# Kernel optimization log

Measured on AMD Instinct MI355X. Metric: run time of the kernel, lower is better.

Reference implementation:

```python
import jax, jax.numpy as jnp
import numpy as np

B, LV, D = 8, 4096, 256   # batch, temporal length, channels
N = 2048                   # total ROIs across the batch
P = 32                     # output_size (number of output bins)
G = int(np.ceil(LV / P))   # static max adaptive sampling grid (sampling_ratio=-1)


def setup_inputs() -> dict:
    key = jax.random.key(0)
    k1, k2, k3 = jax.random.split(key, 3)
    feat = jax.random.normal(k1, (B, LV, D), dtype=jnp.float32)
    # boxes: (start, end) along the lv axis, sorted so start <= end, in [0, LV)
    boxes = jnp.sort(
        jax.random.uniform(k2, (N, 2), dtype=jnp.float32, minval=0.0, maxval=float(LV)),
        axis=1,
    )
    batch_idx = jax.random.randint(k3, (N,), 0, B, dtype=jnp.int32)
    return {"feat": feat, "boxes": boxes, "batch_idx": batch_idx}


def _roi_align_1d(feat, boxes, batch_idx):
    # Faithful 1D specialization of torchvision roi_align with boxes
    # (0, y1, 1, y2), output_size=(P, 1), aligned=True, spatial_scale=1,
    # sampling_ratio=-1. The width axis contributes a single sample at x=0
    # with weight 1, so only the y (lv) axis math remains.
    feat_flat = feat.reshape(B * LV, D)
    y1, y2 = boxes[:, 0], boxes[:, 1]
    roi_h = y2 - y1                       # aligned=True: no max(., 1) clamp
    start = y1 - 0.5                      # aligned offset
    bin_h = roi_h / P                     # [N]
    grid_h = jnp.ceil(bin_h).astype(jnp.int32)          # adaptive samples per bin
    count = jnp.maximum(grid_h, 1).astype(feat.dtype)   # avg denominator
    sub = bin_h / jnp.maximum(grid_h, 1)                # spacing inside a bin [N]
    # bin start positions: [N, P]
    bin_off = start[:, None] + jnp.arange(P, dtype=feat.dtype)[None, :] * bin_h[:, None]
    base = batch_idx.astype(jnp.int32) * LV             # [N] row offset into feat_flat

    def bilinear(y):  # y: [N, P] -> [N, P, D]
        valid = (y >= -1.0) & (y <= float(LV))
        yc = jnp.maximum(y, 0.0)
        y_lo = jnp.floor(yc).astype(jnp.int32)
        hi_case = y_lo >= LV - 1
        y_lo = jnp.where(hi_case, LV - 1, y_lo)
        y_hi = jnp.where(hi_case, LV - 1, y_lo + 1)
        yc = jnp.where(hi_case, y_lo.astype(y.dtype), yc)
        ly = yc - y_lo.astype(y.dtype)
        v = (1.0 - ly)[..., None] * feat_flat[base[:, None] + y_lo] \
            + ly[..., None] * feat_flat[base[:, None] + y_hi]
        return jnp.where(valid[..., None], v, 0.0)

    def step(acc, g):
        y = bin_off + (g.astype(feat.dtype) + 0.5) * sub[:, None]   # [N, P]
        m = (g < grid_h)[:, None, None]                              # sample active?
        return acc + jnp.where(m, bilinear(y), 0.0), None

    acc0 = jnp.zeros((N, P, D), dtype=feat.dtype)
    acc, _ = jax.lax.scan(step, acc0, jnp.arange(G, dtype=jnp.int32))
    return acc / count[:, None, None]   # [N, P, D] (torch output after transpose(1,2))


def reference(feat, boxes, batch_idx):
    return _roi_align_1d(feat, boxes, batch_idx)
```

## Files before the change

### kernel.cpp

```cpp
#include <hip/hip_runtime.h>

#define B_     8
#define LV_    4096
#define D_     256
#define N_     2048
#define P_     32
#define WROWS_ 64
#define SEGS_  4
#define NWIN_  (B_ * (LV_ / WROWS_))
#define NBLK_  (NWIN_ * SEGS_)

typedef float v4f __attribute__((ext_vector_type(4)));

__device__ __forceinline__ float lane_bcast_f(float v, int l) {
    return __int_as_float(__builtin_amdgcn_readlane(__float_as_int(v), l));
}

__device__ __forceinline__ int bin_r_first(const float* __restrict__ boxes, int n, int p) {
    const float y1 = boxes[2 * n], y2 = boxes[2 * n + 1];
    const float bin_h = (y2 - y1) * (1.0f / (float)P_);
    const int gh = (int)ceilf(bin_h);
    if (gh < 1) return 0;
    const float sub  = bin_h / (float)gh;
    const float boff = (y1 - 0.5f) + (float)p * bin_h;
    const float a    = fmaf(0.5f, sub, boff);
    int r = (int)floorf(a);
    if (r < 0) r = 0;
    if (r > LV_ - 1) r = LV_ - 1;
    return r;
}

__global__ __launch_bounds__(256) void build_order_kernel(
    const int* __restrict__ batch_idx, int* __restrict__ order, int* __restrict__ offs)
{
    __shared__ int cnt[B_], cur[B_];
    const int tid = threadIdx.x;
    if (tid < B_) cnt[tid] = 0;
    __syncthreads();
    for (int n = tid; n < N_; n += 256) atomicAdd(&cnt[batch_idx[n]], 1);
    __syncthreads();
    if (tid == 0) {
        int s = 0;
        for (int b = 0; b < B_; ++b) { cur[b] = s; offs[b] = s; s += cnt[b]; }
        offs[B_] = s;
    }
    __syncthreads();
    for (int n = tid; n < N_; n += 256)
        order[atomicAdd(&cur[batch_idx[n]], 1)] = n;
}

__device__ __forceinline__ void process_bin(
    const float* __restrict__ feat, const float* __restrict__ boxes,
    const int* __restrict__ batch_idx, float* __restrict__ out,
    const v4f* tile, int wb, int wlo, int idx, int lane)
{
    const int n = idx >> 5, p = idx & 31;
    const int bi = __builtin_amdgcn_readfirstlane(batch_idx[n]);

    const float y1 = boxes[2 * n], y2 = boxes[2 * n + 1];
    const float bin_h = (y2 - y1) * (1.0f / (float)P_);
    const int gh = (int)ceilf(bin_h);

    const v4f* prow = (const v4f*)feat + (long)bi * (LV_ * (D_ / 4));
    v4f acc0 = {0.f,0.f,0.f,0.f}, acc1 = {0.f,0.f,0.f,0.f};

    if (gh >= 1) {
        const float cntf = (float)gh, sub = bin_h / cntf, inv_sub = 1.0f / sub;
        const float halfsub = 0.5f * sub;
        const float boff = (y1 - 0.5f) + (float)p * bin_h;
        const float a = fmaf(0.5f, sub, boff), ylast = fmaf(cntf - 0.5f, sub, boff);

        int r_first = (int)floorf(a);
        if (r_first < 0) r_first = 0; if (r_first > LV_-1) r_first = LV_-1;
        int r_last = (int)floorf(ylast) + 1;
        if (r_last > LV_-1) r_last = LV_-1; if (r_last < r_first) r_last = r_first;
        const int r0 = __builtin_amdgcn_readfirstlane(r_first);
        const int rl = __builtin_amdgcn_readfirstlane(r_last);
        const float lanef = (float)lane;

        for (int gbase = r0; gbase <= rl; gbase += 64) {
            int kmax = rl - gbase; if (kmax > 63) kmax = 63;

            const int   r  = gbase + lane;
            const float d0 = ((float)gbase + lanef) - a;
            const float dm = d0 - 1.0f, dp = d0 + 1.0f;
            const float nm = fminf(fmaxf(ceilf(dm * inv_sub), 0.0f), cntf);
            const float n0 = fminf(fmaxf(ceilf(d0 * inv_sub), 0.0f), cntf);
            const float np = fminf(fmaxf(ceilf(dp * inv_sub), 0.0f), cntf);
            float Pm = fmaf(nm, dm, -halfsub * fmaf(nm, nm, -nm));
            float P0 = fmaf(n0, d0, -halfsub * fmaf(n0, n0, -n0));
            float Pp = fmaf(np, dp, -halfsub * fmaf(np, np, -np));
            if (r == 0)       Pm = P0;
            if (r == LV_ - 1) Pp = P0 + cntf;
            const float Wl = (Pm + Pp) - 2.0f * P0;

            const int t = kmax + 1;
            int lo, hi;
            if (tile && bi == wb) {
                lo = wlo - gbase;          lo = lo < 0 ? 0 : (lo > t ? t : lo);
                hi = wlo + WROWS_ - gbase; hi = hi < lo ? lo : (hi > t ? t : hi);
            } else { lo = t; hi = t; }

#define GSEG(KS, KE) do {                                                        \
    int k = (KS);                                                                \
    const v4f* pS = prow + (long)(gbase + k) * (D_ / 4);                         \
    for (; k + 4 <= (KE); k += 4) {                                              \
        v4f v0 = pS[lane], v1 = pS[lane+64], v2 = pS[lane+128], v3 = pS[lane+192];\
        acc0 += v0 * lane_bcast_f(Wl, k);   acc1 += v1 * lane_bcast_f(Wl, k+1);  \
        acc0 += v2 * lane_bcast_f(Wl, k+2); acc1 += v3 * lane_bcast_f(Wl, k+3);  \
        pS += 4 * (D_ / 4); }                                                    \
    for (; k < (KE); ++k) { v4f v = pS[lane]; acc0 += v * lane_bcast_f(Wl, k); pS += (D_ / 4); } \
} while (0)

            GSEG(0, lo);
            {
                int k = lo;
                const v4f* tp = tile + (gbase + lo - wlo) * 64 + lane;
                for (; k + 4 <= hi; k += 4) {
                    v4f t0 = tp[0], t1 = tp[64], t2 = tp[128], t3 = tp[192];
                    acc0 += t0 * lane_bcast_f(Wl, k);   acc1 += t1 * lane_bcast_f(Wl, k+1);
                    acc0 += t2 * lane_bcast_f(Wl, k+2); acc1 += t3 * lane_bcast_f(Wl, k+3);
                    tp += 256;
                }
                for (; k < hi; ++k) { acc0 += tp[0] * lane_bcast_f(Wl, k); tp += 64; }
            }
            GSEG(hi, t);
#undef GSEG
        }
    }

    const float inv_c = 1.0f / (float)(gh > 1 ? gh : 1);
    v4f res = (acc0 + acc1) * inv_c;
    v4f* op = (v4f*)out + ((long)n * P_ + p) * (D_ / 4) + lane;
    __builtin_nontemporal_store(res, op);
}

__global__ __launch_bounds__(512) void roi_win_kernel(
    const float* __restrict__ feat, const float* __restrict__ boxes,
    const int* __restrict__ batch_idx, const int* __restrict__ order,
    const int* __restrict__ offs, float* __restrict__ out)
{
    __shared__ v4f tile[WROWS_ * 64];
    __shared__ int flag;

    const int tid  = threadIdx.x;
    const int lane = tid & 63;
    const int wv   = tid >> 6;
    const int bid  = blockIdx.x;

    const int blk = (bid & 7) * (NBLK_ / 8) + (bid >> 3);
    const int w   = blk >> 2;
    const int seg = blk & (SEGS_ - 1);
    const int wb  = w >> 6;
    const int wt  = w & 63;
    const int wlo = wt << 6;

    const int off_b = offs[wb];
    const int cnt_b = offs[wb + 1] - off_b;

    if (tid == 0) flag = 0;
    __syncthreads();
    for (int jj = tid; jj < cnt_b; jj += 512) {
        const int n = order[off_b + jj];
        const int rlo = bin_r_first(boxes, n, 0);
        const int rhi = bin_r_first(boxes, n, P_ - 1);
        if (rlo < wlo + WROWS_ && rhi >= wlo) { flag = 1; break; }
    }
    __syncthreads();
    if (!flag) return;

    {
        const int r0 = wv * 8;
        const float* srow = feat + ((long)wb * LV_ + wlo + r0) * D_ + lane * 4;
        v4f* lrow = tile + r0 * 64;
#if __has_builtin(__builtin_amdgcn_global_load_lds)
        #pragma unroll
        for (int j = 0; j < 8; ++j) {
            __builtin_amdgcn_global_load_lds(
                (const __attribute__((address_space(1))) void*)(srow + j * D_),
                (__attribute__((address_space(3))) void*)(lrow + j * 64),
                16, 0, 0);
        }
#else
        const v4f* src = (const v4f*)feat + ((long)wb * LV_ + wlo + r0) * (D_ / 4) + lane;
        v4f t0 = src[0],   t1 = src[64],  t2 = src[128], t3 = src[192];
        v4f t4 = src[256], t5 = src[320], t6 = src[384], t7 = src[448];
        v4f* dst = lrow + lane;
        dst[0]   = t0; dst[64]  = t1; dst[128] = t2; dst[192] = t3;
        dst[256] = t4; dst[320] = t5; dst[384] = t6; dst[448] = t7;
#endif
    }
    __syncthreads();

    for (int j = seg + SEGS_ * wv; j < cnt_b; j += SEGS_ * 8) {
        const int n = __builtin_amdgcn_readfirstlane(order[off_b + j]);

        const float y1 = boxes[2 * n], y2 = boxes[2 * n + 1];
        const float bin_h = (y2 - y1) * (1.0f / (float)P_);
        const int gh = (int)ceilf(bin_h);

        int pl_c, width;
        if (bin_h > 1e-6f) {
            const float sub   = bin_h / (float)(gh < 1 ? 1 : gh);
            const float A0    = (y1 - 0.5f) + 0.5f * sub;
            const float invbh = 1.0f / bin_h;
            const float plf = (wt == 0)  ? 0.0f  : ((float)wlo - A0) * invbh - 1.0f;
            const float phf = (wt == 63) ? 32.0f : ((float)(wlo + WROWS_) - A0) * invbh + 1.0f;
            int pl = (int)floorf(fminf(fmaxf(plf, 0.0f), 32.0f));
            int ph = (int)ceilf(fminf(fmaxf(phf, 0.0f), 32.0f));
            if (ph < pl) ph = pl;
            pl_c = pl; width = ph - pl;
        } else {
            pl_c = 0; width = 32;
        }
        if (width == 0) continue;

        bool in = false;
        if (lane < width) {
            const int p = pl_c + lane;
            in = ((bin_r_first(boxes, n, p) >> 6) == wt);
        }
        const unsigned long long m = __ballot(in);
        if (!m) continue;
        const int pl   = pl_c + __builtin_ctzll(m);
        const int pcnt = __builtin_popcountll(m);

        for (int pp = pl; pp < pl + pcnt; ++pp)
            process_bin(feat, boxes, batch_idx, out, tile, wb, wlo, (n << 5) | pp, lane);
    }
}

__global__ __launch_bounds__(256) void roi_plain_kernel(
    const float* __restrict__ feat, const float* __restrict__ boxes,
    const int* __restrict__ batch_idx, float* __restrict__ out)
{
    const int slot = blockIdx.x * 4 + (threadIdx.x >> 6);
    const int lane = threadIdx.x & 63;
    process_bin(feat, boxes, batch_idx, out, nullptr, 0, 0, slot, lane);
}

extern "C" void kernel_launch(void* const* d_in, const int* in_sizes, int n_in,
                              void* d_out, int out_size, void* d_ws, size_t ws_size,
                              hipStream_t stream) {
    const float* feat      = (const float*)d_in[0];
    const float* boxes     = (const float*)d_in[1];
    const int*   batch_idx = (const int*)d_in[2];
    float*       out       = (float*)d_out;

    if (ws_size >= (size_t)(N_ + B_ + 1) * sizeof(int)) {
        int* order = (int*)d_ws;
        int* offs  = order + N_;
        build_order_kernel<<<1, 256, 0, stream>>>(batch_idx, order, offs);
        roi_win_kernel<<<NBLK_, 512, 0, stream>>>(feat, boxes, batch_idx, order, offs, out);
    } else {
        roi_plain_kernel<<<(N_ * P_) / 4, 256, 0, stream>>>(feat, boxes, batch_idx, out);
    }
}
```

Measured before the change: 203.6 us.

## Build compacted per-window bin list in LDS for balanced wave scheduling

Each window block now enumerates every (ROI, bin) pair of its batch and counts those whose first sample row lands in the window. It prefix-sums the counts across waves and writes a compact list of bin indices into LDS. Waves then take entries from that list in stride, so work is spread per bin instead of per ROI, replacing the earlier flag prefilter and per-ROI range ballot. The cost is a doubled full scan of 32 bins per ROI for every block, and a fallback global-memory path when the list would exceed its LDS capacity.

```diff
diff --git a/kernel.cpp b/kernel.cpp
--- a/kernel.cpp
+++ b/kernel.cpp
@@ -9,6 +9,7 @@
 #define SEGS_  4
 #define NWIN_  (B_ * (LV_ / WROWS_))
 #define NBLK_  (NWIN_ * SEGS_)
+#define LCAP_  4096
 
 typedef float v4f __attribute__((ext_vector_type(4)));
 
@@ -141,7 +142,8 @@
     const int* __restrict__ offs, float* __restrict__ out)
 {
     __shared__ v4f tile[WROWS_ * 64];
-    __shared__ int flag;
+    __shared__ unsigned short list[LCAP_];
+    __shared__ int wsum[9];
 
     const int tid  = threadIdx.x;
     const int lane = tid & 63;
@@ -155,19 +157,55 @@
     const int wt  = w & 63;
     const int wlo = wt << 6;
 
-    const int off_b = offs[wb];
-    const int cnt_b = offs[wb + 1] - off_b;
-
-    if (tid == 0) flag = 0;
-    __syncthreads();
-    for (int jj = tid; jj < cnt_b; jj += 512) {
-        const int n = order[off_b + jj];
-        const int rlo = bin_r_first(boxes, n, 0);
-        const int rhi = bin_r_first(boxes, n, P_ - 1);
-        if (rlo < wlo + WROWS_ && rhi >= wlo) { flag = 1; break; }
-    }
-    __syncthreads();
-    if (!flag) return;
+    const int off_b  = offs[wb];
+    const int cnt_b  = offs[wb + 1] - off_b;
+    const int npairs = cnt_b * 32;
+
+    int c = 0;
+    for (int q = tid; q < npairs; q += 512) {
+        const int n = order[off_b + (q >> 5)];
+        if ((bin_r_first(boxes, n, q & 31) >> 6) == wt) ++c;
+    }
+    int sc = c;
+    #pragma unroll
+    for (int d = 1; d < 64; d <<= 1) {
+        const int v = __shfl_up(sc, d);
+        if (lane >= d) sc += v;
+    }
+    if (lane == 63) wsum[wv] = sc;
+    __syncthreads();
+    if (tid == 0) {
+        int s = 0;
+        for (int i = 0; i < 8; ++i) { const int t = wsum[i]; wsum[i] = s; s += t; }
+        wsum[8] = s;
+    }
+    __syncthreads();
+    const int K = wsum[8];
+    if (K == 0) return;
+
+    if (K > LCAP_) {
+        const int slot = seg * 8 + wv;
+        for (int j = slot; j < cnt_b; j += 32) {
+            const int n = __builtin_amdgcn_readfirstlane(order[off_b + j]);
+            bool in = false;
+            if (lane < 32) in = ((bin_r_first(boxes, n, lane) >> 6) == wt);
+            unsigned long long m = __ballot(in);
+            while (m) {
+                const int p = __builtin_ctzll(m);
+                m &= m - 1;
+                process_bin(feat, boxes, batch_idx, out, nullptr, 0, 0, (n << 5) | p, lane);
+            }
+        }
+        return;
+    }
+
+    int o = wsum[wv] + (sc - c);
+    for (int q = tid; q < npairs; q += 512) {
+        const int n = order[off_b + (q >> 5)];
+        const int p = q & 31;
+        if ((bin_r_first(boxes, n, p) >> 6) == wt)
+            list[o++] = (unsigned short)((n << 5) | p);
+    }
 
     {
         const int r0 = wv * 8;
@@ -192,41 +230,9 @@
     }
     __syncthreads();
 
-    for (int j = seg + SEGS_ * wv; j < cnt_b; j += SEGS_ * 8) {
-        const int n = __builtin_amdgcn_readfirstlane(order[off_b + j]);
-
-        const float y1 = boxes[2 * n], y2 = boxes[2 * n + 1];
-        const float bin_h = (y2 - y1) * (1.0f / (float)P_);
-        const int gh = (int)ceilf(bin_h);
-
-        int pl_c, width;
-        if (bin_h > 1e-6f) {
-            const float sub   = bin_h / (float)(gh < 1 ? 1 : gh);
-            const float A0    = (y1 - 0.5f) + 0.5f * sub;
-            const float invbh = 1.0f / bin_h;
-            const float plf = (wt == 0)  ? 0.0f  : ((float)wlo - A0) * invbh - 1.0f;
-            const float phf = (wt == 63) ? 32.0f : ((float)(wlo + WROWS_) - A0) * invbh + 1.0f;
-            int pl = (int)floorf(fminf(fmaxf(plf, 0.0f), 32.0f));
-            int ph = (int)ceilf(fminf(fmaxf(phf, 0.0f), 32.0f));
-            if (ph < pl) ph = pl;
-            pl_c = pl; width = ph - pl;
-        } else {
-            pl_c = 0; width = 32;
-        }
-        if (width == 0) continue;
-
-        bool in = false;
-        if (lane < width) {
-            const int p = pl_c + lane;
-            in = ((bin_r_first(boxes, n, p) >> 6) == wt);
-        }
-        const unsigned long long m = __ballot(in);
-        if (!m) continue;
-        const int pl   = pl_c + __builtin_ctzll(m);
-        const int pcnt = __builtin_popcountll(m);
-
-        for (int pp = pl; pp < pl + pcnt; ++pp)
-            process_bin(feat, boxes, batch_idx, out, tile, wb, wlo, (n << 5) | pp, lane);
+    for (int i = seg + 4 * wv; i < K; i += SEGS_ * 8) {
+        const int idx = __builtin_amdgcn_readfirstlane((int)list[i]);
+        process_bin(feat, boxes, batch_idx, out, tile, wb, wlo, idx, lane);
     }
 }
 
```

Result: slower. 208.7 us (+2.5%).
